# Kernel tuning notes

Measured on AMD Instinct MI355X. Metric: run time of the kernel, lower is better.

## Reference

```python
import jax, jax.numpy as jnp
import numpy as np

N = 4096
D = 1024          # latent_vector_size
H, KD, VD = 16, 64, 64
MHK = H * KD      # 1024
MHV = H * VD      # 1024
HID = D // 2      # 512
EPS = 1e-5


def _layernorm(v, g, b):
    mu = jnp.mean(v, axis=-1, keepdims=True)
    var = jnp.mean(jnp.square(v - mu), axis=-1, keepdims=True)
    return (v - mu) * jax.lax.rsqrt(var + EPS) * g + b


def setup_inputs() -> dict:
    key = jax.random.key(0)
    ks = jax.random.split(key, 12)
    s = lambda fan_in: 1.0 / np.sqrt(fan_in)
    return {
        "x": jax.random.normal(ks[0], (N, D), dtype=jnp.float32),
        "w_qkv": jax.random.uniform(ks[1], (D, H * (2 * KD + VD)), jnp.float32, -s(D), s(D)),
        "b_qkv": jax.random.uniform(ks[2], (H * (2 * KD + VD),), jnp.float32, -s(D), s(D)),
        "w_msa": jax.random.uniform(ks[3], (MHV, D), jnp.float32, -s(MHV), s(MHV)),
        "b_msa": jax.random.uniform(ks[4], (D,), jnp.float32, -s(MHV), s(MHV)),
        "ln_g": jnp.ones((D,), jnp.float32),
        "ln_b": jnp.zeros((D,), jnp.float32),
        "w_h1": jax.random.uniform(ks[5], (D, HID), jnp.float32, -s(D), s(D)),
        "b_h1": jax.random.uniform(ks[6], (HID,), jnp.float32, -s(D), s(D)),
        "w_h2": jax.random.uniform(ks[7], (HID, D), jnp.float32, -s(HID), s(HID)),
        "b_h2": jax.random.uniform(ks[8], (D,), jnp.float32, -s(HID), s(HID)),
    }


def reference(x, w_qkv, b_qkv, w_msa, b_msa, ln_g, ln_b, w_h1, b_h1, w_h2, b_h2):
    # --- attention block (note: heads are never split; one big [N,N] softmax) ---
    ln1 = _layernorm(x, ln_g, ln_b)                       # [N, D]
    qkv = ln1 @ w_qkv + b_qkv                             # [N, 3*MHK]
    q, k, v = qkv[:, :MHK], qkv[:, MHK:2 * MHK], qkv[:, 2 * MHK:]
    scores = (q @ k.T) / jnp.sqrt(jnp.float32(KD))        # [N, N]
    attn = jax.nn.softmax(scores, axis=-1)
    mha = (attn @ v) @ w_msa + b_msa                      # [N, D]
    enc1 = x + mha
    # --- MLP block (shared layernorm params; softmax output, residual) ---
    ln2 = _layernorm(enc1, ln_g, ln_b)
    h1 = jax.nn.gelu(ln2 @ w_h1 + b_h1, approximate=False)  # [N, HID]
    h2 = jax.nn.gelu(h1 @ w_h2 + b_h2, approximate=False)   # [N, D]
    out = jax.nn.softmax(h2, axis=-1)                        # nn.Softmax() -> dim=1 for 2D
    return enc1 + out
```

## Files before the change

kernel.cpp:

```cpp
#include <hip/hip_runtime.h>
#include <stdint.h>

#define DEV __device__ __forceinline__

typedef unsigned short u16;
typedef __attribute__((ext_vector_type(8))) unsigned short u16x8;
typedef __attribute__((ext_vector_type(8))) short s16x8;
typedef __attribute__((ext_vector_type(4))) unsigned short u16x4;
typedef __attribute__((ext_vector_type(4))) float f32x4;

DEV float bf2f(u16 u) { return __uint_as_float(((unsigned)u) << 16); }
DEV u16 f2bf(float f) {
  unsigned u = __float_as_uint(f);
  u += 0x7FFFu + ((u >> 16) & 1u);
  return (u16)(u >> 16);
}
DEV float gelu_exact(float v) { return 0.5f * v * (1.0f + erff(v * 0.70710678118654752f)); }

#define BARF asm volatile("s_barrier" ::: "memory")

__global__ __launch_bounds__(256) void transpose4_f32_bf16(
    const float* __restrict__ wqkv, u16* __restrict__ wqkvT,
    const float* __restrict__ wmsa, u16* __restrict__ wmsaT,
    const float* __restrict__ wh1, u16* __restrict__ wh1T,
    const float* __restrict__ wh2, u16* __restrict__ wh2T) {
  __shared__ float t[32][33];
  const int id = blockIdx.x;
  const float* in; u16* out; int rows, cols, bx, by;
  if (id < 3072)      { in = wqkv; out = wqkvT; rows = 1024; cols = 3072; bx = id % 96;          by = id / 96; }
  else if (id < 4096) { in = wmsa; out = wmsaT; rows = 1024; cols = 1024; bx = (id - 3072) % 32; by = (id - 3072) / 32; }
  else if (id < 4608) { in = wh1;  out = wh1T;  rows = 1024; cols = 512;  bx = (id - 4096) % 16; by = (id - 4096) / 16; }
  else                { in = wh2;  out = wh2T;  rows = 512;  cols = 1024; bx = (id - 4608) % 32; by = (id - 4608) / 32; }
  const int tx = threadIdx.x, ty = threadIdx.y;
  const int c0 = bx * 32, r0 = by * 32;
#pragma unroll
  for (int i = 0; i < 32; i += 8) t[ty + i][tx] = in[(size_t)(r0 + ty + i) * cols + c0 + tx];
  __syncthreads();
#pragma unroll
  for (int i = 0; i < 32; i += 8)
    out[(size_t)(c0 + ty + i) * rows + r0 + tx] = f2bf(t[tx][ty + i]);
}

__global__ __launch_bounds__(256) void transpose_bf16(
    const u16* __restrict__ in, int ldin, u16* __restrict__ out, int ldout) {
  __shared__ u16 t[32][33];
  const int tx = threadIdx.x, ty = threadIdx.y;
  const int c0 = blockIdx.x * 32, r0 = blockIdx.y * 32;
#pragma unroll
  for (int i = 0; i < 32; i += 8) t[ty + i][tx] = in[(size_t)(r0 + ty + i) * ldin + c0 + tx];
  __syncthreads();
#pragma unroll
  for (int i = 0; i < 32; i += 8)
    out[(size_t)(c0 + ty + i) * ldout + r0 + tx] = t[tx][ty + i];
}

__global__ __launch_bounds__(256) void layernorm_bf16(
    const float* __restrict__ in, const float* __restrict__ g,
    const float* __restrict__ b, u16* __restrict__ out) {
  const int tid = threadIdx.x;
  const int lane = tid & 63, wid = tid >> 6;
  const size_t base = (size_t)blockIdx.x * 1024;
  const float4 v = ((const float4*)(in + base))[tid];
  float s = v.x + v.y + v.z + v.w;
  float ss = v.x * v.x + v.y * v.y + v.z * v.z + v.w * v.w;
#pragma unroll
  for (int off = 32; off > 0; off >>= 1) {
    s += __shfl_down(s, off);
    ss += __shfl_down(ss, off);
  }
  __shared__ float red[8];
  if (lane == 0) { red[wid] = s; red[4 + wid] = ss; }
  __syncthreads();
  s = red[0] + red[1] + red[2] + red[3];
  ss = red[4] + red[5] + red[6] + red[7];
  const float mu = s * (1.0f / 1024.0f);
  const float inv = rsqrtf(ss * (1.0f / 1024.0f) - mu * mu + 1e-5f);
  const float4 gv = ((const float4*)g)[tid];
  const float4 bv = ((const float4*)b)[tid];
  u16x4 o;
  o.x = f2bf((v.x - mu) * inv * gv.x + bv.x);
  o.y = f2bf((v.y - mu) * inv * gv.y + bv.y);
  o.z = f2bf((v.z - mu) * inv * gv.z + bv.z);
  o.w = f2bf((v.w - mu) * inv * gv.w + bv.w);
  *(u16x4*)(out + base + tid * 4) = o;
}

__global__ __launch_bounds__(256) void softmax4096(u16* __restrict__ p) {
  const int tid = threadIdx.x;
  const int lane = tid & 63, wid = tid >> 6;
  u16* row = p + (size_t)blockIdx.x * 4096;
  u16x8 r0 = ((u16x8*)row)[tid * 2];
  u16x8 r1 = ((u16x8*)row)[tid * 2 + 1];
  float v[16];
#pragma unroll
  for (int i = 0; i < 8; ++i) { v[i] = bf2f(r0[i]); v[8 + i] = bf2f(r1[i]); }
  float mx = v[0];
#pragma unroll
  for (int i = 1; i < 16; ++i) mx = fmaxf(mx, v[i]);
#pragma unroll
  for (int off = 32; off > 0; off >>= 1) mx = fmaxf(mx, __shfl_down(mx, off));
  __shared__ float red[8];
  if (lane == 0) red[wid] = mx;
  __syncthreads();
  mx = fmaxf(fmaxf(red[0], red[1]), fmaxf(red[2], red[3]));
  float sum = 0.0f;
#pragma unroll
  for (int i = 0; i < 16; ++i) { v[i] = __expf(v[i] - mx); sum += v[i]; }
#pragma unroll
  for (int off = 32; off > 0; off >>= 1) sum += __shfl_down(sum, off);
  if (lane == 0) red[4 + wid] = sum;
  __syncthreads();
  sum = red[4] + red[5] + red[6] + red[7];
  const float inv = 1.0f / sum;
  u16x8 o0, o1;
#pragma unroll
  for (int i = 0; i < 8; ++i) { o0[i] = f2bf(v[i] * inv); o1[i] = f2bf(v[8 + i] * inv); }
  ((u16x8*)row)[tid * 2] = o0;
  ((u16x8*)row)[tid * 2 + 1] = o1;
}

__global__ __launch_bounds__(256) void final_softmax_add(
    const float* __restrict__ h2, const float* __restrict__ enc1, float* __restrict__ out) {
  const int tid = threadIdx.x;
  const int lane = tid & 63, wid = tid >> 6;
  const size_t base = (size_t)blockIdx.x * 1024;
  float4 v = ((const float4*)(h2 + base))[tid];
  float mx = fmaxf(fmaxf(v.x, v.y), fmaxf(v.z, v.w));
#pragma unroll
  for (int off = 32; off > 0; off >>= 1) mx = fmaxf(mx, __shfl_down(mx, off));
  __shared__ float red[8];
  if (lane == 0) red[wid] = mx;
  __syncthreads();
  mx = fmaxf(fmaxf(red[0], red[1]), fmaxf(red[2], red[3]));
  v.x = __expf(v.x - mx); v.y = __expf(v.y - mx);
  v.z = __expf(v.z - mx); v.w = __expf(v.w - mx);
  float sum = v.x + v.y + v.z + v.w;
#pragma unroll
  for (int off = 32; off > 0; off >>= 1) sum += __shfl_down(sum, off);
  if (lane == 0) red[4 + wid] = sum;
  __syncthreads();
  sum = red[4] + red[5] + red[6] + red[7];
  const float inv = 1.0f / sum;
  const float4 e = ((const float4*)(enc1 + base))[tid];
  float4 o;
  o.x = e.x + v.x * inv; o.y = e.y + v.y * inv;
  o.z = e.z + v.z * inv; o.w = e.w + v.w * inv;
  ((float4*)(out + base))[tid] = o;
}

__global__ __launch_bounds__(256) void reduce_partials(
    const u16* __restrict__ P, u16* __restrict__ out) {
  const size_t i = ((size_t)blockIdx.x * 256 + threadIdx.x) * 8;
  const size_t S = 4096ull * 1024ull;
  u16x8 p0 = *(const u16x8*)(P + i);
  u16x8 p1 = *(const u16x8*)(P + S + i);
  u16x8 p2 = *(const u16x8*)(P + 2 * S + i);
  u16x8 p3 = *(const u16x8*)(P + 3 * S + i);
  u16x8 o;
#pragma unroll
  for (int j = 0; j < 8; ++j)
    o[j] = f2bf(bf2f(p0[j]) + bf2f(p1[j]) + bf2f(p2[j]) + bf2f(p3[j]));
  *(u16x8*)(out + i) = o;
}

template <int EPI>
__global__ __launch_bounds__(512, 4) void gemm256k32(
    const u16* __restrict__ A, int lda, const u16* __restrict__ Bt, int ldb,
    u16* __restrict__ C, int ldc, const float* __restrict__ bias, float scale,
    int K, int nsplit, size_t sliceStride) {
  __shared__ alignas(16) u16 As[2][256 * 32];
  __shared__ alignas(16) u16 Bs[2][128 * 32];
  const int tid = threadIdx.x;
  const int lane = tid & 63;
  const int wid = tid >> 6;
  const int wr = wid >> 1, wc = wid & 1;

  const int gx = gridDim.x;
  const int nwg = gx * gridDim.y;
  int wg = blockIdx.y * gx + blockIdx.x;
  wg = (wg & 7) * (nwg >> 3) + (wg >> 3);
  const int by = wg / gx;
  const int bxk = wg % gx;
  const int ks = bxk % nsplit;
  const int bx = bxk / nsplit;
  const int m0 = by * 256, n0 = bx * 128;
  A += (size_t)ks * K;
  Bt += (size_t)ks * K;
  C += (size_t)ks * sliceStride;

  const u16* Apan = A + (size_t)m0 * lda;
  const u16* Bpan = Bt + (size_t)n0 * ldb;

  const int srow = lane >> 2;
  const int sseg = ((lane & 3) ^ ((lane >> 3) & 3)) * 8;
  const int koff = (((lane >> 4) ^ ((lane >> 1) & 3))) * 8;

  f32x4 acc[4][4];
#pragma unroll
  for (int m = 0; m < 4; ++m)
#pragma unroll
    for (int n = 0; n < 4; ++n) { f32x4 z = {0.f, 0.f, 0.f, 0.f}; acc[m][n] = z; }

  const int arow = wr * 64 + (lane & 15);
  const int brow = wc * 64 + (lane & 15);

  auto STAGE = [&](int S, int t) {
#pragma unroll
    for (int i = 0; i < 2; ++i) {
      const int rbase = i * 128 + wid * 16;
      const u16* ga = Apan + (size_t)(rbase + srow) * lda + t * 32 + sseg;
      __builtin_amdgcn_global_load_lds((const __attribute__((address_space(1))) void*)ga,
                                       (__attribute__((address_space(3))) void*)&As[S][rbase * 32],
                                       16, 0, 0);
    }
    const int rbase = wid * 16;
    const u16* gb = Bpan + (size_t)(rbase + srow) * ldb + t * 32 + sseg;
    __builtin_amdgcn_global_load_lds((const __attribute__((address_space(1))) void*)gb,
                                     (__attribute__((address_space(3))) void*)&Bs[S][rbase * 32],
                                     16, 0, 0);
  };

  const int NT = K >> 5;

  STAGE(0, 0);
  asm volatile("s_waitcnt vmcnt(0)" ::: "memory");
  BARF;

  int s = 0;
  for (int t = 0; t < NT; ++t) {
    if (t + 1 < NT) STAGE(s ^ 1, t + 1);

    s16x8 a[4], b[4];
#pragma unroll
    for (int m = 0; m < 4; ++m) a[m] = *(const s16x8*)&As[s][(arow + m * 16) * 32 + koff];
#pragma unroll
    for (int n = 0; n < 4; ++n) b[n] = *(const s16x8*)&Bs[s][(brow + n * 16) * 32 + koff];
#pragma unroll
    for (int m = 0; m < 4; ++m)
#pragma unroll
      for (int n = 0; n < 4; ++n)
        acc[m][n] = __builtin_amdgcn_mfma_f32_16x16x32_bf16(a[m], b[n], acc[m][n], 0, 0, 0);

    asm volatile("s_waitcnt vmcnt(0)" ::: "memory");
    BARF;
    s ^= 1;
  }

  const int crow0 = m0 + wr * 64 + ((lane >> 4) << 2);
  const int ccol0 = n0 + wc * 64 + (lane & 15);
#pragma unroll
  for (int m = 0; m < 4; ++m) {
#pragma unroll
    for (int n = 0; n < 4; ++n) {
      const int col = ccol0 + n * 16;
      float bia = 0.0f;
      if (EPI == 1) bia = bias[col];
#pragma unroll
      for (int r = 0; r < 4; ++r) {
        const int row = crow0 + m * 16 + r;
        float v = acc[m][n][r];
        if (EPI == 0) v *= scale;
        if (EPI == 1) v += bia;
        C[(size_t)row * ldc + col] = f2bf(v);
      }
    }
  }
}

template <int EPI>
__global__ __launch_bounds__(256) void gemm_bt(
    const u16* __restrict__ A, int lda, const u16* __restrict__ Bt, int ldb,
    void* __restrict__ Cv, int ldc, const float* __restrict__ bias,
    const float* __restrict__ xres, int ldx, float scale, int K) {
  __shared__ alignas(16) u16 As[3][128 * 32];
  __shared__ alignas(16) u16 Bs[3][128 * 32];
  const int tid = threadIdx.x;
  const int wid = tid >> 6;
  const int lane = tid & 63;

  const int gx = gridDim.x;
  const int nwg = gridDim.x * gridDim.y;
  int wg = blockIdx.y * gx + blockIdx.x;
  wg = (wg & 7) * (nwg >> 3) + (wg >> 3);
  const int m0 = (wg / gx) * 128;
  const int n0 = (wg % gx) * 128;
  const int wr = wid >> 1, wc = wid & 1;

  const int srow = lane >> 2;
  const int sseg = (((lane & 3) ^ ((lane >> 3) & 3))) * 8;

  f32x4 acc[4][4];
#pragma unroll
  for (int m = 0; m < 4; ++m)
#pragma unroll
    for (int n = 0; n < 4; ++n) { f32x4 z = {0.f, 0.f, 0.f, 0.f}; acc[m][n] = z; }

  const int arow = wr * 64 + (lane & 15);
  const int brow = wc * 64 + (lane & 15);
  const int koff = (((lane >> 4) ^ ((lane >> 1) & 3))) * 8;

  const int NT = K >> 5;

  auto STAGE = [&](int kt, int buf) {
    const int k0 = kt * 32;
#pragma unroll
    for (int i = 0; i < 2; ++i) {
      const int r = i * 64 + wid * 16;
      const u16* ga = A + (size_t)(m0 + r + srow) * lda + k0 + sseg;
      const u16* gb = Bt + (size_t)(n0 + r + srow) * ldb + k0 + sseg;
      __builtin_amdgcn_global_load_lds((const __attribute__((address_space(1))) void*)ga,
                                       (__attribute__((address_space(3))) void*)&As[buf][r * 32], 16, 0, 0);
      __builtin_amdgcn_global_load_lds((const __attribute__((address_space(1))) void*)gb,
                                       (__attribute__((address_space(3))) void*)&Bs[buf][r * 32], 16, 0, 0);
    }
  };

  STAGE(0, 0);
  STAGE(1, 1);
  asm volatile("s_waitcnt vmcnt(4)" ::: "memory");
  BARF;

  int cur = 0;
  for (int t = 0; t < NT; ++t) {
    const int kt = (t + 2 < NT) ? (t + 2) : (NT - 1);
    STAGE(kt, (cur + 2) % 3);

    s16x8 a[4], b[4];
#pragma unroll
    for (int m = 0; m < 4; ++m) a[m] = *(const s16x8*)&As[cur][(arow + m * 16) * 32 + koff];
#pragma unroll
    for (int n = 0; n < 4; ++n) b[n] = *(const s16x8*)&Bs[cur][(brow + n * 16) * 32 + koff];
#pragma unroll
    for (int m = 0; m < 4; ++m)
#pragma unroll
      for (int n = 0; n < 4; ++n)
        acc[m][n] = __builtin_amdgcn_mfma_f32_16x16x32_bf16(a[m], b[n], acc[m][n], 0, 0, 0);

    asm volatile("s_waitcnt vmcnt(4)" ::: "memory");
    BARF;
    cur = (cur + 1) % 3;
  }

  const int crow0 = m0 + wr * 64 + ((lane >> 4) << 2);
  const int ccol0 = n0 + wc * 64 + (lane & 15);
#pragma unroll
  for (int m = 0; m < 4; ++m) {
#pragma unroll
    for (int n = 0; n < 4; ++n) {
      const int col = ccol0 + n * 16;
      const float bia = bias[col];
#pragma unroll
      for (int r = 0; r < 4; ++r) {
        const int row = crow0 + m * 16 + r;
        const float v = acc[m][n][r];
        if (EPI == 3) {
          ((float*)Cv)[(size_t)row * ldc + col] = v + bia + xres[(size_t)row * ldx + col];
        } else if (EPI == 4) {
          ((u16*)Cv)[(size_t)row * ldc + col] = f2bf(gelu_exact(v + bia));
        } else {
          ((float*)Cv)[(size_t)row * ldc + col] = gelu_exact(v + bia);
        }
      }
    }
  }
  (void)scale;
}

extern "C" void kernel_launch(void* const* d_in, const int* in_sizes, int n_in,
                              void* d_out, int out_size, void* d_ws, size_t ws_size,
                              hipStream_t stream) {
  const float* x     = (const float*)d_in[0];
  const float* w_qkv = (const float*)d_in[1];
  const float* b_qkv = (const float*)d_in[2];
  const float* w_msa = (const float*)d_in[3];
  const float* b_msa = (const float*)d_in[4];
  const float* ln_g  = (const float*)d_in[5];
  const float* ln_b  = (const float*)d_in[6];
  const float* w_h1  = (const float*)d_in[7];
  const float* b_h1  = (const float*)d_in[8];
  const float* w_h2  = (const float*)d_in[9];
  const float* b_h2  = (const float*)d_in[10];

  char* w = (char*)d_ws;
  u16*   qkv   = (u16*)(w + 0);
  u16*   sc    = (u16*)(w + 25165824);
  u16*   lnb   = (u16*)(w + 58720256);
  u16*   av    = (u16*)(w + 67108864);
  u16*   vT    = (u16*)(w + 75497472);
  float* enc1  = (float*)(w + 83886080);
  u16*   part  = (u16*)(w + 83886080);
  u16*   h1    = (u16*)(w + 100663296);
  float* h2    = (float*)(w + 104857600);
  u16*   wqkvT = (u16*)(w + 121634816);
  u16*   wmsaT = (u16*)(w + 127926272);
  u16*   wh1T  = (u16*)(w + 130023424);
  u16*   wh2T  = (u16*)(w + 131072000);
  (void)in_sizes; (void)n_in; (void)out_size; (void)ws_size;

  dim3 tb(32, 8);
  transpose4_f32_bf16<<<5120, tb, 0, stream>>>(w_qkv, wqkvT, w_msa, wmsaT,
                                               w_h1, wh1T, w_h2, wh2T);

  layernorm_bf16<<<4096, 256, 0, stream>>>(x, ln_g, ln_b, lnb);
  gemm256k32<1><<<dim3(24, 16), 512, 0, stream>>>(lnb, 1024, wqkvT, 1024, qkv, 3072,
                                                  b_qkv, 1.0f, 1024, 1, 0);
  transpose_bf16<<<dim3(32, 128), tb, 0, stream>>>(qkv + 2048, 3072, vT, 4096);
  gemm256k32<0><<<dim3(32, 16), 512, 0, stream>>>(qkv, 3072, qkv + 1024, 3072, sc, 4096,
                                                  nullptr, 0.125f, 1024, 1, 0);
  softmax4096<<<4096, 256, 0, stream>>>(sc);
  gemm256k32<2><<<dim3(32, 16), 512, 0, stream>>>(sc, 4096, vT, 4096, part, 1024,
                                                  nullptr, 1.0f, 1024, 4, 4096ull * 1024ull);
  reduce_partials<<<2048, 256, 0, stream>>>(part, av);
  gemm_bt<3><<<dim3(8, 32), 256, 0, stream>>>(av, 1024, wmsaT, 1024, enc1, 1024,
                                              b_msa, x, 1024, 1.0f, 1024);
  layernorm_bf16<<<4096, 256, 0, stream>>>(enc1, ln_g, ln_b, lnb);
  gemm_bt<4><<<dim3(4, 32), 256, 0, stream>>>(lnb, 1024, wh1T, 1024, h1, 512,
                                              b_h1, nullptr, 0, 1.0f, 1024);
  gemm_bt<5><<<dim3(8, 32), 256, 0, stream>>>(h1, 512, wh2T, 512, h2, 1024,
                                              b_h2, nullptr, 0, 1.0f, 512);
  final_softmax_add<<<4096, 256, 0, stream>>>(h2, enc1, (float*)d_out);
}
```

Before: 246.7 us.

## Load B operand directly from K-packed global layout into registers, K=64 tiles

Reworks the three big attention GEMMs so the B operand is prepacked in a k-major layout of 8-element chunks and read straight from global memory into registers, double-buffered, instead of being staged through LDS. The A tile grows to K=64 with an XOR swizzle, and the MFMA block runs at raised wave priority. New kpack/vpack kernels build the packed K and V, and the QKV weight is packed during the initial weight conversion. This is meant to cut LDS traffic and barriers per k-step, at the cost of more VGPRs (occupancy hint lowered to 2), extra packing launches, and uncoalesced-looking strided B loads that rely on L2.

```diff
diff --git a/kernel.cpp b/kernel.cpp
--- a/kernel.cpp
+++ b/kernel.cpp
@@ -20,14 +20,14 @@
 #define BARF asm volatile("s_barrier" ::: "memory")
 
 __global__ __launch_bounds__(256) void transpose4_f32_bf16(
-    const float* __restrict__ wqkv, u16* __restrict__ wqkvT,
+    const float* __restrict__ wqkv, u16* __restrict__ wqkvP,
     const float* __restrict__ wmsa, u16* __restrict__ wmsaT,
     const float* __restrict__ wh1, u16* __restrict__ wh1T,
     const float* __restrict__ wh2, u16* __restrict__ wh2T) {
   __shared__ float t[32][33];
   const int id = blockIdx.x;
-  const float* in; u16* out; int rows, cols, bx, by;
-  if (id < 3072)      { in = wqkv; out = wqkvT; rows = 1024; cols = 3072; bx = id % 96;          by = id / 96; }
+  const float* in; u16* out; int rows, cols, bx, by; int packed = 0;
+  if (id < 3072)      { in = wqkv; out = wqkvP; rows = 1024; cols = 3072; bx = id % 96;          by = id / 96; packed = 1; }
   else if (id < 4096) { in = wmsa; out = wmsaT; rows = 1024; cols = 1024; bx = (id - 3072) % 32; by = (id - 3072) / 32; }
   else if (id < 4608) { in = wh1;  out = wh1T;  rows = 1024; cols = 512;  bx = (id - 4096) % 16; by = (id - 4096) / 16; }
   else                { in = wh2;  out = wh2T;  rows = 512;  cols = 1024; bx = (id - 4608) % 32; by = (id - 4608) / 32; }
@@ -36,22 +36,39 @@
 #pragma unroll
   for (int i = 0; i < 32; i += 8) t[ty + i][tx] = in[(size_t)(r0 + ty + i) * cols + c0 + tx];
   __syncthreads();
-#pragma unroll
-  for (int i = 0; i < 32; i += 8)
-    out[(size_t)(c0 + ty + i) * rows + r0 + tx] = f2bf(t[tx][ty + i]);
-}
-
-__global__ __launch_bounds__(256) void transpose_bf16(
-    const u16* __restrict__ in, int ldin, u16* __restrict__ out, int ldout) {
-  __shared__ u16 t[32][33];
+  if (packed) {
+    const int k = r0 + tx;
+#pragma unroll
+    for (int i = 0; i < 32; i += 8) {
+      const int n = c0 + ty + i;
+      out[((size_t)(k >> 3) * cols + n) * 8 + (k & 7)] = f2bf(t[tx][ty + i]);
+    }
+  } else {
+#pragma unroll
+    for (int i = 0; i < 32; i += 8)
+      out[(size_t)(c0 + ty + i) * rows + r0 + tx] = f2bf(t[tx][ty + i]);
+  }
+}
+
+__global__ __launch_bounds__(256) void kpack(const u16* __restrict__ qkv, u16* __restrict__ kp) {
+  const int idx = blockIdx.x * 256 + threadIdx.x;
+  const int row = idx >> 7, kseg = idx & 127;
+  u16x8 v = *(const u16x8*)(qkv + (size_t)row * 3072 + 1024 + kseg * 8);
+  *(u16x8*)(kp + ((size_t)kseg * 4096 + row) * 8) = v;
+}
+
+__global__ __launch_bounds__(256) void vpack(const u16* __restrict__ qkv, u16* __restrict__ vp) {
+  __shared__ u16 t[64][33];
   const int tx = threadIdx.x, ty = threadIdx.y;
-  const int c0 = blockIdx.x * 32, r0 = blockIdx.y * 32;
-#pragma unroll
-  for (int i = 0; i < 32; i += 8) t[ty + i][tx] = in[(size_t)(r0 + ty + i) * ldin + c0 + tx];
-  __syncthreads();
-#pragma unroll
-  for (int i = 0; i < 32; i += 8)
-    out[(size_t)(c0 + ty + i) * ldout + r0 + tx] = t[tx][ty + i];
+  const int v0 = blockIdx.x * 32, t0 = blockIdx.y * 64;
+#pragma unroll
+  for (int j = 0; j < 8; ++j)
+    t[ty * 8 + j][tx] = qkv[(size_t)(t0 + ty * 8 + j) * 3072 + 2048 + v0 + tx];
+  __syncthreads();
+  u16x8 w;
+#pragma unroll
+  for (int j = 0; j < 8; ++j) w[j] = t[ty * 8 + j][tx];
+  *(u16x8*)(vp + ((size_t)(t0 / 8 + ty) * 1024 + (v0 + tx)) * 8) = w;
 }
 
 __global__ __launch_bounds__(256) void layernorm_bf16(
@@ -164,12 +181,11 @@
 }
 
 template <int EPI>
-__global__ __launch_bounds__(512, 4) void gemm256k32(
-    const u16* __restrict__ A, int lda, const u16* __restrict__ Bt, int ldb,
+__global__ __launch_bounds__(512, 2) void gemm_bd(
+    const u16* __restrict__ A, int lda, const u16* __restrict__ Bp, int Nb,
     u16* __restrict__ C, int ldc, const float* __restrict__ bias, float scale,
     int K, int nsplit, size_t sliceStride) {
-  __shared__ alignas(16) u16 As[2][256 * 32];
-  __shared__ alignas(16) u16 Bs[2][128 * 32];
+  __shared__ alignas(16) u16 As[2][256 * 64];
   const int tid = threadIdx.x;
   const int lane = tid & 63;
   const int wid = tid >> 6;
@@ -185,15 +201,16 @@
   const int bx = bxk / nsplit;
   const int m0 = by * 256, n0 = bx * 128;
   A += (size_t)ks * K;
-  Bt += (size_t)ks * K;
+  Bp += (size_t)ks * (size_t)(K >> 3) * (size_t)Nb * 8;
   C += (size_t)ks * sliceStride;
 
   const u16* Apan = A + (size_t)m0 * lda;
-  const u16* Bpan = Bt + (size_t)n0 * ldb;
-
-  const int srow = lane >> 2;
-  const int sseg = ((lane & 3) ^ ((lane >> 3) & 3)) * 8;
-  const int koff = (((lane >> 4) ^ ((lane >> 1) & 3))) * 8;
+  const size_t bstrideK = (size_t)Nb * 8;
+  const int hi4 = lane >> 4;
+  const u16* Bcol = Bp + (size_t)(n0 + wc * 64 + (lane & 15)) * 8;
+
+  const int sgk = ((lane & 7) ^ ((lane >> 3) & 7)) * 8;
+  const int arow_e = (wr * 64 + (lane & 15)) * 64;
 
   f32x4 acc[4][4];
 #pragma unroll
@@ -201,52 +218,67 @@
 #pragma unroll
     for (int n = 0; n < 4; ++n) { f32x4 z = {0.f, 0.f, 0.f, 0.f}; acc[m][n] = z; }
 
-  const int arow = wr * 64 + (lane & 15);
-  const int brow = wc * 64 + (lane & 15);
-
-  auto STAGE = [&](int S, int t) {
-#pragma unroll
-    for (int i = 0; i < 2; ++i) {
-      const int rbase = i * 128 + wid * 16;
-      const u16* ga = Apan + (size_t)(rbase + srow) * lda + t * 32 + sseg;
-      __builtin_amdgcn_global_load_lds((const __attribute__((address_space(1))) void*)ga,
-                                       (__attribute__((address_space(3))) void*)&As[S][rbase * 32],
-                                       16, 0, 0);
+  s16x8 b0[4][2], b1[4][2];
+
+  auto STAGE_A = [&](int t, int s) {
+#pragma unroll
+    for (int i = 0; i < 4; ++i) {
+      const int rbase = i * 64 + wid * 8;
+      const int row = rbase + (lane >> 3);
+      const u16* src = Apan + (size_t)row * lda + t * 64 + sgk;
+      __builtin_amdgcn_global_load_lds(
+          (const __attribute__((address_space(1))) void*)src,
+          (__attribute__((address_space(3))) void*)(&As[s][0] + rbase * 64 + lane * 8),
+          16, 0, 0);
     }
-    const int rbase = wid * 16;
-    const u16* gb = Bpan + (size_t)(rbase + srow) * ldb + t * 32 + sseg;
-    __builtin_amdgcn_global_load_lds((const __attribute__((address_space(1))) void*)gb,
-                                     (__attribute__((address_space(3))) void*)&Bs[S][rbase * 32],
-                                     16, 0, 0);
   };
 
-  const int NT = K >> 5;
-
-  STAGE(0, 0);
-  asm volatile("s_waitcnt vmcnt(0)" ::: "memory");
-  BARF;
-
-  int s = 0;
-  for (int t = 0; t < NT; ++t) {
-    if (t + 1 < NT) STAGE(s ^ 1, t + 1);
-
-    s16x8 a[4], b[4];
-#pragma unroll
-    for (int m = 0; m < 4; ++m) a[m] = *(const s16x8*)&As[s][(arow + m * 16) * 32 + koff];
-#pragma unroll
-    for (int n = 0; n < 4; ++n) b[n] = *(const s16x8*)&Bs[s][(brow + n * 16) * 32 + koff];
+  auto LOADB = [&](int t, s16x8 (&bn)[4][2]) {
+#pragma unroll
+    for (int n = 0; n < 4; ++n)
+#pragma unroll
+      for (int kk = 0; kk < 2; ++kk)
+        bn[n][kk] = *(const s16x8*)(Bcol + (size_t)(t * 8 + kk * 4 + hi4) * bstrideK + n * 128);
+  };
+
+  const int NT = K >> 6;
+
+  auto BODY = [&](int t, int s, s16x8 (&bc)[4][2], s16x8 (&bn)[4][2]) {
+    const int tn = (t + 1 < NT) ? t + 1 : NT - 1;
+    STAGE_A(tn, s ^ 1);
+    LOADB(tn, bn);
+    asm volatile("s_waitcnt vmcnt(12)" ::: "memory");
+    BARF;
+    s16x8 a[4][2];
 #pragma unroll
     for (int m = 0; m < 4; ++m)
 #pragma unroll
+      for (int kk = 0; kk < 2; ++kk)
+        a[m][kk] = *(const s16x8*)&As[s][arow_e + m * 16 * 64 +
+                                         (((kk * 4 + hi4) ^ (lane & 7)) * 8)];
+    __builtin_amdgcn_s_setprio(1);
+#pragma unroll
+    for (int m = 0; m < 4; ++m)
+#pragma unroll
       for (int n = 0; n < 4; ++n)
-        acc[m][n] = __builtin_amdgcn_mfma_f32_16x16x32_bf16(a[m], b[n], acc[m][n], 0, 0, 0);
-
-    asm volatile("s_waitcnt vmcnt(0)" ::: "memory");
+#pragma unroll
+        for (int kk = 0; kk < 2; ++kk)
+          acc[m][n] = __builtin_amdgcn_mfma_f32_16x16x32_bf16(a[m][kk], bc[n][kk],
+                                                              acc[m][n], 0, 0, 0);
+    __builtin_amdgcn_s_setprio(0);
+    asm volatile("s_waitcnt lgkmcnt(0)" ::: "memory");
     BARF;
-    s ^= 1;
-  }
-
-  const int crow0 = m0 + wr * 64 + ((lane >> 4) << 2);
+  };
+
+  STAGE_A(0, 0);
+  LOADB(0, b0);
+
+  for (int it = 0; it < (NT >> 1); ++it) {
+    BODY(2 * it, 0, b0, b1);
+    BODY(2 * it + 1, 1, b1, b0);
+  }
+
+  const int crow0 = m0 + wr * 64 + (hi4 << 2);
   const int ccol0 = n0 + wc * 64 + (lane & 15);
 #pragma unroll
   for (int m = 0; m < 4; ++m) {
@@ -385,31 +417,33 @@
   u16*   qkv   = (u16*)(w + 0);
   u16*   sc    = (u16*)(w + 25165824);
   u16*   lnb   = (u16*)(w + 58720256);
+  u16*   vp    = (u16*)(w + 58720256);
   u16*   av    = (u16*)(w + 67108864);
-  u16*   vT    = (u16*)(w + 75497472);
+  u16*   kp    = (u16*)(w + 75497472);
   float* enc1  = (float*)(w + 83886080);
   u16*   part  = (u16*)(w + 83886080);
   u16*   h1    = (u16*)(w + 100663296);
   float* h2    = (float*)(w + 104857600);
-  u16*   wqkvT = (u16*)(w + 121634816);
+  u16*   wqkvP = (u16*)(w + 121634816);
   u16*   wmsaT = (u16*)(w + 127926272);
   u16*   wh1T  = (u16*)(w + 130023424);
   u16*   wh2T  = (u16*)(w + 131072000);
   (void)in_sizes; (void)n_in; (void)out_size; (void)ws_size;
 
   dim3 tb(32, 8);
-  transpose4_f32_bf16<<<5120, tb, 0, stream>>>(w_qkv, wqkvT, w_msa, wmsaT,
+  transpose4_f32_bf16<<<5120, tb, 0, stream>>>(w_qkv, wqkvP, w_msa, wmsaT,
                                                w_h1, wh1T, w_h2, wh2T);
 
   layernorm_bf16<<<4096, 256, 0, stream>>>(x, ln_g, ln_b, lnb);
-  gemm256k32<1><<<dim3(24, 16), 512, 0, stream>>>(lnb, 1024, wqkvT, 1024, qkv, 3072,
-                                                  b_qkv, 1.0f, 1024, 1, 0);
-  transpose_bf16<<<dim3(32, 128), tb, 0, stream>>>(qkv + 2048, 3072, vT, 4096);
-  gemm256k32<0><<<dim3(32, 16), 512, 0, stream>>>(qkv, 3072, qkv + 1024, 3072, sc, 4096,
-                                                  nullptr, 0.125f, 1024, 1, 0);
+  gemm_bd<1><<<dim3(24, 16), 512, 0, stream>>>(lnb, 1024, wqkvP, 3072, qkv, 3072,
+                                               b_qkv, 1.0f, 1024, 1, 0);
+  kpack<<<2048, 256, 0, stream>>>(qkv, kp);
+  vpack<<<dim3(32, 64), tb, 0, stream>>>(qkv, vp);
+  gemm_bd<0><<<dim3(32, 16), 512, 0, stream>>>(qkv, 3072, kp, 4096, sc, 4096,
+                                               nullptr, 0.125f, 1024, 1, 0);
   softmax4096<<<4096, 256, 0, stream>>>(sc);
-  gemm256k32<2><<<dim3(32, 16), 512, 0, stream>>>(sc, 4096, vT, 4096, part, 1024,
-                                                  nullptr, 1.0f, 1024, 4, 4096ull * 1024ull);
+  gemm_bd<2><<<dim3(32, 16), 512, 0, stream>>>(sc, 4096, vp, 1024, part, 1024,
+                                               nullptr, 1.0f, 1024, 4, 4096ull * 1024ull);
   reduce_partials<<<2048, 256, 0, stream>>>(part, av);
   gemm_bt<3><<<dim3(8, 32), 256, 0, stream>>>(av, 1024, wmsaT, 1024, enc1, 1024,
                                               b_msa, x, 1024, 1.0f, 1024);
```

Result: slower. 292.4 us (+18.5%).
